# Kernel tuning notes

Measured on AMD Instinct MI355X. Metric: run time of the kernel, lower is better.

The kernel has to match this reference:

```python
import jax, jax.numpy as jnp
import numpy as np

_BN_EPS = 1e-5


def _conv2d(x, w, b, dilation):
    # x: (B,C,T,F), w: (O,I,k,k); 'same' padding per DilatedConv: (k-1)*d//2
    k = w.shape[-1]
    pad = (k - 1) * dilation // 2
    y = jax.lax.conv_general_dilated(
        x, w, window_strides=(1, 1),
        padding=[(pad, pad), (pad, pad)],
        rhs_dilation=(dilation, dilation),
        dimension_numbers=('NCHW', 'OIHW', 'NCHW'))
    return y + b[None, :, None, None]


def _gate(x, w, b, gamma, beta, mean, var, dilation):
    # conv -> BatchNorm2d (inference) -> chunk -> tanh * sigmoid
    y = _conv2d(x, w, b, dilation)
    scale = gamma * jax.lax.rsqrt(var + _BN_EPS)
    y = (y - mean[None, :, None, None]) * scale[None, :, None, None] + beta[None, :, None, None]
    a, g = jnp.split(y, 2, axis=1)
    return jnp.tanh(a) * jax.nn.sigmoid(g)


def _gru(x, wih, whh, bih, bhh):
    # forward-direction GRU (PyTorch gate order r,z,n). x: (T,N,I) -> (T,N,H)
    H = whh.shape[-1]
    gi = jnp.einsum('tni,hi->tnh', x, wih) + bih  # (T,N,3H), input projections

    def step(h, gi_t):
        gh = h @ whh.T + bhh
        r = jax.nn.sigmoid(gi_t[:, :H] + gh[:, :H])
        z = jax.nn.sigmoid(gi_t[:, H:2 * H] + gh[:, H:2 * H])
        n = jnp.tanh(gi_t[:, 2 * H:] + r * gh[:, 2 * H:])
        h_new = (1.0 - z) * n + z * h
        return h_new, h_new

    h0 = jnp.zeros((x.shape[1], H), x.dtype)
    _, ys = jax.lax.scan(step, h0, gi)
    return ys


def setup_inputs() -> dict:
    key = jax.random.key(0)
    ks = jax.random.split(key, 32)
    B, T, F, C, G = 8, 512, 256, 16, 8
    Cg = C // G  # 2
    d = {'x': jax.random.normal(ks[0], (B, 2, T, F), jnp.float32)}
    ki = 1
    for name, cin in zip(('g1', 'g2', 'g3', 'g4'), (2, C, C, C)):
        d[name + '_w'] = jax.random.normal(ks[ki], (2 * C, cin, 3, 3), jnp.float32) * (0.5 / np.sqrt(cin * 9.0)); ki += 1
        d[name + '_b'] = jax.random.normal(ks[ki], (2 * C,), jnp.float32) * 0.05; ki += 1
        d[name + '_gamma'] = 1.0 + 0.1 * jax.random.normal(ks[ki], (2 * C,), jnp.float32); ki += 1
        d[name + '_beta'] = 0.1 * jax.random.normal(ks[ki], (2 * C,), jnp.float32); ki += 1
        d[name + '_mean'] = jnp.zeros((2 * C,), jnp.float32)
        d[name + '_var'] = jnp.ones((2 * C,), jnp.float32)
    d['gru_wih'] = jax.random.normal(ks[ki], (G, 3 * Cg, Cg), jnp.float32) * 0.3; ki += 1
    d['gru_whh'] = jax.random.normal(ks[ki], (G, 3 * Cg, Cg), jnp.float32) * 0.3; ki += 1
    d['gru_bih'] = jax.random.normal(ks[ki], (G, 3 * Cg), jnp.float32) * 0.1; ki += 1
    d['gru_bhh'] = jax.random.normal(ks[ki], (G, 3 * Cg), jnp.float32) * 0.1; ki += 1
    d['out_w'] = jax.random.normal(ks[ki], (1, C), jnp.float32) * 0.3; ki += 1
    d['out_b'] = jax.random.normal(ks[ki], (1,), jnp.float32) * 0.05
    return d


def reference(x, g1_w, g1_b, g1_gamma, g1_beta, g1_mean, g1_var,
              g2_w, g2_b, g2_gamma, g2_beta, g2_mean, g2_var,
              g3_w, g3_b, g3_gamma, g3_beta, g3_mean, g3_var,
              g4_w, g4_b, g4_gamma, g4_beta, g4_mean, g4_var,
              gru_wih, gru_whh, gru_bih, gru_bhh, out_w, out_b):
    out = _gate(x, g1_w, g1_b, g1_gamma, g1_beta, g1_mean, g1_var, 1)
    out = _gate(out, g2_w, g2_b, g2_gamma, g2_beta, g2_mean, g2_var, 2)
    out = _gate(out, g3_w, g3_b, g3_gamma, g3_beta, g3_mean, g3_var, 4)
    out = _gate(out, g4_w, g4_b, g4_gamma, g4_beta, g4_mean, g4_var, 8)
    B, C, T, F = out.shape
    G = gru_wih.shape[0]
    Cg = C // G
    # split channels into G groups of Cg, run GRU over time, batched over (B*F)
    xg = out.reshape(B, G, Cg, T, F).transpose(1, 3, 0, 4, 2).reshape(G, T, B * F, Cg)
    ys = jax.vmap(_gru)(xg, gru_wih, gru_whh, gru_bih, gru_bhh)  # (G,T,B*F,Cg)
    merged = ys.reshape(G, T, B, F, Cg).transpose(2, 0, 4, 1, 3).reshape(B, C, T, F)
    # 1x1 out_conv -> 1 channel
    return jnp.einsum('bctf,oc->botf', merged, out_w) + out_b[None, :, None, None]
```

## Files before the change

kernel.cpp:

```cpp
#include <hip/hip_runtime.h>

#define Bb 8
#define Tt 512
#define Ff 256
#define Cc 16
#define TF (Tt*Ff)
#define TROW 528
#define FROW 272
#define CELL 32
#define WROWB (144*CELL)
#define BUFBYTES ((size_t)Bb*TROW*FROW*CELL)

typedef _Float16 half8 __attribute__((ext_vector_type(8)));
typedef __attribute__((ext_vector_type(4))) float f32x4;

typedef const __attribute__((address_space(1))) void* gas1_t;
typedef __attribute__((address_space(3))) void* las3_t;
#define GLOAD_LDS(g, l) __builtin_amdgcn_global_load_lds((gas1_t)(const void*)(g), (las3_t)(void*)(l), 16, 0, 0)

#define WAIT_VM8  0x0F78
#define WAIT_VM24 0x4F78
#define WAIT_VM40 0x8F78

__device__ __forceinline__ float fexp2(float x) { return __builtin_amdgcn_exp2f(x); }

__device__ __forceinline__ float fast_sigmoid(float x) {
    return __builtin_amdgcn_rcpf(1.0f + fexp2(-1.4426950408889634f * x));
}
__device__ __forceinline__ float fast_tanh(float x) {
    return 1.0f - 2.0f * __builtin_amdgcn_rcpf(fexp2(2.8853900817779268f * x) + 1.0f);
}

__device__ __forceinline__ unsigned short hbits(float x) {
    _Float16 h = (_Float16)x;
    return __builtin_bit_cast(unsigned short, h);
}
__device__ __forceinline__ float h2f(unsigned short u) {
    return (float)__builtin_bit_cast(_Float16, u);
}
__device__ __forceinline__ f32x4 mfma_f16(half8 a, half8 b, f32x4 c) {
    return __builtin_amdgcn_mfma_f32_16x16x32_f16(a, b, c, 0, 0, 0);
}
__device__ __forceinline__ float dpp_swap8(float x) {
    int xi = __builtin_bit_cast(int, x);
    int r = __builtin_amdgcn_mov_dpp(xi, 0x128, 0xf, 0xf, true);
    return __builtin_bit_cast(float, r);
}

__global__ __launch_bounds__(256)
void setup_all(const float* __restrict__ x1, const float* __restrict__ w1, const float* __restrict__ b1,
               const float* __restrict__ gm1, const float* __restrict__ bt1,
               const float* __restrict__ mn1, const float* __restrict__ vr1,
               const float* __restrict__ w2, const float* __restrict__ b2, const float* __restrict__ gm2,
               const float* __restrict__ bt2, const float* __restrict__ mn2, const float* __restrict__ vr2,
               const float* __restrict__ w3, const float* __restrict__ b3, const float* __restrict__ gm3,
               const float* __restrict__ bt3, const float* __restrict__ mn3, const float* __restrict__ vr3,
               const float* __restrict__ w4, const float* __restrict__ b4, const float* __restrict__ gm4,
               const float* __restrict__ bt4, const float* __restrict__ mn4, const float* __restrict__ vr4,
               char* __restrict__ bufA, char* __restrict__ bufB,
               char* __restrict__ wpreAll, float* __restrict__ bpreAll)
{
    const int blk = blockIdx.x;
    const int tid = threadIdx.x;
    if (blk < 3) {
        const float *w, *bias, *gamma, *beta, *mean, *var;
        if (blk == 0)      { w = w2; bias = b2; gamma = gm2; beta = bt2; mean = mn2; var = vr2; }
        else if (blk == 1) { w = w3; bias = b3; gamma = gm3; beta = bt3; mean = mn3; var = vr3; }
        else               { w = w4; bias = b4; gamma = gm4; beta = bt4; mean = mn4; var = vr4; }
        char* wpre = wpreAll + blk * 20480;
        float* bpre = bpreAll + blk * 32;
        if (tid < 32) {
            float s = gamma[tid] * rsqrtf(var[tid] + 1e-5f);
            bpre[tid] = (bias[tid] - mean[tid]) * s + beta[tid];
        }
        for (int i = tid; i < 4608; i += 256) {
            int co = i / 144, r = i - co * 144;
            int ci = r / 9, tap = r - ci * 9;
            float s = gamma[co] * rsqrtf(var[co] + 1e-5f);
            float wv = w[(co * 16 + ci) * 9 + tap] * s;
            unsigned short hi = hbits(wv);
            unsigned short lo = hbits((wv - h2f(hi)) * 2048.0f);
            int ks = tap >> 1, tp = tap & 1;
            int kl = tp * 16 + ci;
            int qq = kl >> 3, jj = kl & 7;
            int sub = qq ^ (co & 3);
            *(unsigned short*)(wpre + ((0 * 5 + ks) * 32 + co) * 64 + sub * 16 + jj * 2) = hi;
            *(unsigned short*)(wpre + ((1 * 5 + ks) * 32 + co) * 64 + sub * 16 + jj * 2) = lo;
        }
        for (int i = tid; i < 1024; i += 256) {
            int p = i >> 9, rem = i & 511;
            int co = rem >> 4, kl = 16 + (rem & 15);
            int qq = kl >> 3, jj = kl & 7;
            int sub = qq ^ (co & 3);
            *(unsigned short*)(wpre + ((p * 5 + 4) * 32 + co) * 64 + sub * 16 + jj * 2) = 0;
        }
    } else if (blk < 787) {
        int idx = (blk - 3) * 256 + tid;
        int which = idx >= 100352;
        int r0 = which ? idx - 100352 : idx;
        int b = r0 / 12544, c = r0 - b * 12544;
        int tp, fp;
        if (c < 4352) { int row = c / 272; fp = c - row * 272; tp = row < 8 ? row : 512 + row; }
        else { int c2 = c - 4352; tp = 8 + (c2 >> 4); int fi = c2 & 15; fp = fi < 8 ? fi : 256 + fi; }
        char* base = (which ? bufB : bufA) + ((size_t)(b * TROW + tp) * FROW + fp) * CELL;
        float4 z = make_float4(0.f, 0.f, 0.f, 0.f);
        float4* p = (float4*)base;
        p[0] = z; p[1] = z;
    } else {
        __shared__ float xs[2][6][66];
        __shared__ float wl[18 * 32];
        __shared__ float bnsL[32], bnoL[32];
        int bb = blk - 787;
        int fx = bb & 3;
        int ty = (bb >> 2) & 127;
        int b  = bb >> 9;
        const int f0 = fx * 64;
        const int t0 = ty * 4;
        const int fl = tid & 63;
        const int tr = (tid >> 6) & 1;
        const int h  = tid >> 7;

        if (tid < 32) {
            float s = gm1[tid] * rsqrtf(vr1[tid] + 1e-5f);
            bnsL[tid] = s;
            bnoL[tid] = (b1[tid] - mn1[tid]) * s + bt1[tid];
        }
        for (int i = tid; i < 576; i += 256) {
            int co = i & 31, rest = i >> 5;
            int ci = rest / 9, tap = rest - ci * 9;
            wl[rest * 32 + co] = w1[(co * 2 + ci) * 9 + tap];
        }
        for (int i = tid; i < 792; i += 256) {
            int ci = i / 396, r = i - ci * 396;
            int row = r / 66, col = r - row * 66;
            int t_in = t0 + row - 1, f_in = f0 + col - 1;
            float v = 0.f;
            if (t_in >= 0 && t_in < Tt && f_in >= 0 && f_in < Ff)
                v = x1[((size_t)(b * 2 + ci) * Tt + t_in) * Ff + f_in];
            xs[ci][row][col] = v;
        }
        __syncthreads();

        float acc[2][16];
        #pragma unroll
        for (int q = 0; q < 2; q++)
            #pragma unroll
            for (int j = 0; j < 16; j++) acc[q][j] = 0.f;

        #pragma unroll
        for (int ci = 0; ci < 2; ci++) {
            float win[4][3];
            #pragma unroll
            for (int r = 0; r < 4; r++)
                #pragma unroll
                for (int c = 0; c < 3; c++)
                    win[r][c] = xs[ci][2 * tr + r][fl + c];
            #pragma unroll
            for (int dt = 0; dt < 3; dt++)
                #pragma unroll
                for (int kf = 0; kf < 3; kf++) {
                    float xv0 = win[dt][kf];
                    float xv1 = win[dt + 1][kf];
                    const float* wrow = wl + (ci * 9 + dt * 3 + kf) * 32 + h * 8;
                    float wv[16];
                    *(float4*)(wv)      = *(const float4*)(wrow);
                    *(float4*)(wv + 4)  = *(const float4*)(wrow + 4);
                    *(float4*)(wv + 8)  = *(const float4*)(wrow + 16);
                    *(float4*)(wv + 12) = *(const float4*)(wrow + 20);
                    #pragma unroll
                    for (int j = 0; j < 16; j++) {
                        acc[0][j] = fmaf(xv0, wv[j], acc[0][j]);
                        acc[1][j] = fmaf(xv1, wv[j], acc[1][j]);
                    }
                }
        }

        #pragma unroll
        for (int q = 0; q < 2; q++) {
            int t = t0 + 2 * tr + q;
            int fp = f0 + fl + 8;
            int sw = fp & 1;
            char* cell = bufA + ((size_t)(b * TROW + t + 8) * FROW + fp) * CELL;
            unsigned short hv[8];
            #pragma unroll
            for (int j = 0; j < 8; j++) {
                int ca = h * 8 + j, cg = 16 + h * 8 + j;
                float av = acc[q][j]     * bnsL[ca] + bnoL[ca];
                float gv = acc[q][8 + j] * bnsL[cg] + bnoL[cg];
                hv[j] = hbits(fast_tanh(av) * fast_sigmoid(gv));
            }
            uint4 P;
            P.x = (unsigned)hv[0] | ((unsigned)hv[1] << 16);
            P.y = (unsigned)hv[2] | ((unsigned)hv[3] << 16);
            P.z = (unsigned)hv[4] | ((unsigned)hv[5] << 16);
            P.w = (unsigned)hv[6] | ((unsigned)hv[7] << 16);
            *(uint4*)(cell + ((h ^ sw) * 16)) = P;
        }
    }
}

template<int DIL, int WRITE_F32>
__global__ __launch_bounds__(256, 2)
void gate_mfma(const char* __restrict__ actIn, const char* __restrict__ wpre,
               const float* __restrict__ bpre, char* __restrict__ outBuf)
{
    __shared__ char actL[32768];
    const int tg = blockIdx.x, fh = blockIdx.y, b = blockIdx.z;
    const int tid = threadIdx.x;
    const int w = tid >> 6, lane = tid & 63;
    const int n = lane & 15, q = lane >> 4;
    const int tsel = w >> 1, fsel = w & 1;
    constexpr int GPC = 128 / DIL;
    const int rcl = tg / GPC, m = tg - rcl * GPC;
    const int t0 = rcl + 4 * m * DIL;
    const int f0 = fh * 128;

    half8 aH[5][2], aL[5][2];
    #pragma unroll
    for (int ks = 0; ks < 5; ks++)
        #pragma unroll
        for (int ct = 0; ct < 2; ct++) {
            int co = ct * 16 + n;
            int sub = q ^ (co & 3);
            aH[ks][ct] = *(const half8*)(wpre + (size_t)((0 * 5 + ks) * 32 + co) * 64 + sub * 16);
            aL[ks][ct] = *(const half8*)(wpre + (size_t)((5 + ks) * 32 + co) * 64 + sub * 16);
        }

    #pragma unroll
    for (int i = 0; i < 6; i++) {
        int tp = t0 + 8 + (i - 1) * DIL;
        const char* src = actIn + ((size_t)(b * TROW + tp) * FROW + f0) * CELL;
        char* dst = actL + i * WROWB;
        GLOAD_LDS(src + tid * 16, dst + tid * 16);
        if (tid < 64)
            GLOAD_LDS(src + (224 + tid) * 16, dst + (224 + tid) * 16);
    }
    __syncthreads();

    const int fbl = fsel * 64;
    f32x4 accH[2][4][2] = {}, accL[2][4][2] = {};

    #pragma unroll
    for (int ks = 0; ks < 5; ks++) {
        const int tapA = 2 * ks;
        const int tapB = (2 * ks + 1 > 8) ? 8 : 2 * ks + 1;
        const int rowA = tapA / 3, dfA = (tapA % 3 - 1) * DIL;
        const int rowB = tapB / 3, dfB = (tapB % 3 - 1) * DIL;
        int tapSel = q >> 1;
        int rowt = tapSel ? rowB : rowA;
        int df  = tapSel ? dfB : dfA;
        int cih = q & 1;
        #pragma unroll
        for (int tj = 0; tj < 2; tj++) {
            const int jj = 2 * tsel + tj;
            const char* rbase = actL + (jj + rowt) * WROWB;
            #pragma unroll
            for (int nt = 0; nt < 4; nt++) {
                int fp = 8 + fbl + nt * 16 + n + df;
                const char* cell = rbase + fp * CELL;
                half8 bF = *(const half8*)(cell + ((cih ^ (fp & 1)) * 16));
                #pragma unroll
                for (int ct = 0; ct < 2; ct++) {
                    accH[tj][nt][ct] = mfma_f16(aH[ks][ct], bF, accH[tj][nt][ct]);
                    accL[tj][nt][ct] = mfma_f16(aL[ks][ct], bF, accL[tj][nt][ct]);
                }
            }
        }
    }

    float4 bA = *(const float4*)(bpre + q * 4);
    float4 bG = *(const float4*)(bpre + 16 + q * 4);
    const float CL = 4.8828125e-4f;
    __syncthreads();

    if (WRITE_F32) {
        float* Ef = (float*)actL;
        #pragma unroll
        for (int tj = 0; tj < 2; tj++) {
            const int jj = 2 * tsel + tj;
            #pragma unroll
            for (int nt = 0; nt < 4; nt++) {
                float a0 = accH[tj][nt][0].x + CL * accL[tj][nt][0].x + bA.x;
                float a1 = accH[tj][nt][0].y + CL * accL[tj][nt][0].y + bA.y;
                float a2 = accH[tj][nt][0].z + CL * accL[tj][nt][0].z + bA.z;
                float a3 = accH[tj][nt][0].w + CL * accL[tj][nt][0].w + bA.w;
                float g0 = accH[tj][nt][1].x + CL * accL[tj][nt][1].x + bG.x;
                float g1 = accH[tj][nt][1].y + CL * accL[tj][nt][1].y + bG.y;
                float g2 = accH[tj][nt][1].z + CL * accL[tj][nt][1].z + bG.z;
                float g3 = accH[tj][nt][1].w + CL * accL[tj][nt][1].w + bG.w;
                float r[4];
                r[0] = fast_tanh(a0) * fast_sigmoid(g0);
                r[1] = fast_tanh(a1) * fast_sigmoid(g1);
                r[2] = fast_tanh(a2) * fast_sigmoid(g2);
                r[3] = fast_tanh(a3) * fast_sigmoid(g3);
                int fl = fbl + nt * 16 + n;
                #pragma unroll
                for (int j = 0; j < 4; j++)
                    Ef[(jj * 16 + q * 4 + j) * 128 + fl] = r[j];
            }
        }
        __syncthreads();
        float* gp = (float*)outBuf;
        #pragma unroll
        for (int k = 0; k < 8; k++) {
            int linear = k * 256 + tid;
            int jj2 = linear >> 9;
            int rem = linear & 511;
            int c = rem >> 5, fq = rem & 31;
            int tt = t0 + jj2 * DIL;
            *(float4*)(gp + (size_t)(b * 16 + c) * TF + tt * Ff + fh * 128 + fq * 4) =
                *(const float4*)(Ef + (jj2 * 16 + c) * 128 + fq * 4);
        }
    } else {
        char* Eo = actL;
        #pragma unroll
        for (int tj = 0; tj < 2; tj++) {
            const int jj = 2 * tsel + tj;
            #pragma unroll
            for (int nt = 0; nt < 4; nt++) {
                float a0 = accH[tj][nt][0].x + CL * accL[tj][nt][0].x + bA.x;
                float a1 = accH[tj][nt][0].y + CL * accL[tj][nt][0].y + bA.y;
                float a2 = accH[tj][nt][0].z + CL * accL[tj][nt][0].z + bA.z;
                float a3 = accH[tj][nt][0].w + CL * accL[tj][nt][0].w + bA.w;
                float g0 = accH[tj][nt][1].x + CL * accL[tj][nt][1].x + bG.x;
                float g1 = accH[tj][nt][1].y + CL * accL[tj][nt][1].y + bG.y;
                float g2 = accH[tj][nt][1].z + CL * accL[tj][nt][1].z + bG.z;
                float g3 = accH[tj][nt][1].w + CL * accL[tj][nt][1].w + bG.w;
                unsigned short hv[4];
                hv[0] = hbits(fast_tanh(a0) * fast_sigmoid(g0));
                hv[1] = hbits(fast_tanh(a1) * fast_sigmoid(g1));
                hv[2] = hbits(fast_tanh(a2) * fast_sigmoid(g2));
                hv[3] = hbits(fast_tanh(a3) * fast_sigmoid(g3));
                int fl = fbl + nt * 16 + n;
                int sw = (fh * 128 + fl + 8) & 1;
                uint2 pk;
                pk.x = (unsigned)hv[0] | ((unsigned)hv[1] << 16);
                pk.y = (unsigned)hv[2] | ((unsigned)hv[3] << 16);
                char* base = Eo + (jj * 128 + fl) * CELL;
                *(uint2*)(base + ((q >> 1) ^ sw) * 16 + (q & 1) * 8) = pk;
            }
        }
        __syncthreads();
        #pragma unroll
        for (int k = 0; k < 4; k++) {
            int linear = k * 256 + tid;
            int jj2 = linear >> 8;
            int idx = linear & 255;
            int tt = t0 + jj2 * DIL;
            char* dstRow = outBuf + ((size_t)(b * TROW + tt + 8) * FROW + fh * 128 + 8) * CELL;
            *(uint4*)(dstRow + idx * 16) = *(const uint4*)(Eo + jj2 * 4096 + idx * 16);
        }
    }
}

__global__ __launch_bounds__(128)
void gru_kernel(const float* __restrict__ xin, const float* __restrict__ wih,
                const float* __restrict__ whh, const float* __restrict__ bih,
                const float* __restrict__ bhh, const float* __restrict__ out_w,
                float* __restrict__ part)
{
    __shared__ float ldsF[2][3 * 2048];
    const int tid = threadIdx.x;
    const int wv = tid >> 6, lane = tid & 63;
    const int b = blockIdx.x >> 5;
    const int g = (blockIdx.x >> 2) & 7;
    const int fblk = (blockIdx.x & 3) * 2 + wv;
    const int f0 = fblk * 32;

    const int row = lane >> 4;
    const int u = (lane >> 3) & 1;
    const int fi = (lane & 7) | (row << 3);

    const float L2E = 1.4426950408889634f;
    float Wi0[3], Wi1[3], Whs[3], Who[3], Bi[3], Bh[3];
    #pragma unroll
    for (int p = 0; p < 3; p++) {
        int rw = p * 2 + u;
        Wi0[p] = wih[g * 12 + rw * 2 + 0] * L2E;
        Wi1[p] = wih[g * 12 + rw * 2 + 1] * L2E;
        Whs[p] = whh[g * 12 + rw * 2 + u] * L2E;
        Who[p] = whh[g * 12 + rw * 2 + (1 - u)] * L2E;
        Bi[p]  = bih[g * 6 + rw] * L2E;
        Bh[p]  = bhh[g * 6 + rw] * L2E;
    }
    const float ow = out_w[2 * g + u];

    const int s = lane & 7, cch = (lane >> 3) & 1, trr = lane >> 4;
    const float* gsrc = xin + ((size_t)(b * Cc + 2 * g + cch) * Tt + trr) * Ff + f0 + s * 4;
    float* ldsW = ldsF[wv];

    float* poW = part + ((((size_t)(b * 8 + g) * 8 + fblk) * 256) * 128) + u * 64 + fi * 2;

    #define STAGE(bsel, chunk)                                                 \
    {                                                                          \
        char* ldst = (char*)(ldsW + (bsel) * 2048) + lane * 16;                \
        const float* gs = gsrc + (size_t)(chunk) * 32 * Ff;                    \
        _Pragma("unroll")                                                      \
        for (int i = 0; i < 8; i++)                                            \
            GLOAD_LDS(gs + i * 4 * Ff, ldst + i * 1024);                       \
    }

    float h = 0.f;
    STAGE(0, 0); STAGE(1, 1);

    for (int k = 0; k < 16; k++) {
        __builtin_amdgcn_sched_barrier(0);
        if (k == 0)      __builtin_amdgcn_s_waitcnt(WAIT_VM8);
        else if (k == 1) __builtin_amdgcn_s_waitcnt(WAIT_VM24);
        else             __builtin_amdgcn_s_waitcnt(WAIT_VM40);
        __builtin_amdgcn_sched_barrier(0);
        int bc = k - (k / 3) * 3;
        const float* cbase = ldsW + bc * 2048;
        float2 outR[16];
        #pragma unroll
        for (int tt = 0; tt < 32; tt++) {
            const float* cell = cbase + (tt >> 2) * 256 + (tt & 3) * 64;
            float x0 = cell[fi];
            float x1 = cell[32 + fi];
            float ho = dpp_swap8(h);
            float gir = fmaf(Wi1[0], x1, fmaf(Wi0[0], x0, Bi[0]));
            float giz = fmaf(Wi1[1], x1, fmaf(Wi0[1], x0, Bi[1]));
            float gin = fmaf(Wi1[2], x1, fmaf(Wi0[2], x0, Bi[2]));
            float ghr = fmaf(Who[0], ho, fmaf(Whs[0], h, Bh[0]));
            float ghz = fmaf(Who[1], ho, fmaf(Whs[1], h, Bh[1]));
            float ghn = fmaf(Who[2], ho, fmaf(Whs[2], h, Bh[2]));
            float r = __builtin_amdgcn_rcpf(1.f + fexp2(-(gir + ghr)));
            float z = __builtin_amdgcn_rcpf(1.f + fexp2(-(giz + ghz)));
            float an = fmaf(r, ghn, gin);
            float nv = fmaf(-2.f, __builtin_amdgcn_rcpf(fexp2(an + an) + 1.f), 1.f);
            h = fmaf(z, h - nv, nv);
            float o = h * ow;
            if (tt & 1) outR[tt >> 1].y = o; else outR[tt >> 1].x = o;
        }
        int cs = k + 2; cs &= 15;
        int bs = k + 2; bs -= (bs / 3) * 3;
        STAGE(bs, cs);
        #pragma unroll
        for (int j = 0; j < 16; j++)
            *(float2*)(poW + (k * 16 + j) * 128) = outR[j];
    }
    #undef STAGE
}

__global__ __launch_bounds__(256)
void out_kernel(const float* __restrict__ part, const float* __restrict__ out_b,
                float* __restrict__ out)
{
    int idx = blockIdx.x * 256 + threadIdx.x;
    int f = idx & 255;
    int tp = (idx >> 8) & 255;
    int b = idx >> 16;
    int fsl = f >> 5, fi = f & 31;
    const float* base = part + (size_t)b * 2097152 + (size_t)fsl * 32768 + tp * 128 + fi * 2;
    float ob = out_b[0];
    float s0 = ob, s1 = ob;
    #pragma unroll
    for (int g = 0; g < 8; g++)
        #pragma unroll
        for (int u = 0; u < 2; u++) {
            float2 v = *(const float2*)(base + (size_t)g * 262144 + u * 64);
            s0 += v.x; s1 += v.y;
        }
    float* op = out + ((size_t)b * Tt + 2 * tp) * Ff + f;
    op[0] = s0;
    op[Ff] = s1;
}

extern "C" void kernel_launch(void* const* d_in, const int* in_sizes, int n_in,
                              void* d_out, int out_size, void* d_ws, size_t ws_size,
                              hipStream_t stream) {
    char* bufA = (char*)d_ws;
    char* bufB = bufA + BUFBYTES;
    float* gruF = (float*)(bufB + BUFBYTES);
    char* wpre = (char*)gruF + (size_t)Bb * Cc * TF * 4;
    float* bpre = (float*)(wpre + 3 * 20480);
    float* partF = (float*)bufA;

    setup_all<<<787 + 4096, 256, 0, stream>>>(
        (const float*)d_in[0],
        (const float*)d_in[1],  (const float*)d_in[2],  (const float*)d_in[3],
        (const float*)d_in[4],  (const float*)d_in[5],  (const float*)d_in[6],
        (const float*)d_in[7],  (const float*)d_in[8],  (const float*)d_in[9],
        (const float*)d_in[10], (const float*)d_in[11], (const float*)d_in[12],
        (const float*)d_in[13], (const float*)d_in[14], (const float*)d_in[15],
        (const float*)d_in[16], (const float*)d_in[17], (const float*)d_in[18],
        (const float*)d_in[19], (const float*)d_in[20], (const float*)d_in[21],
        (const float*)d_in[22], (const float*)d_in[23], (const float*)d_in[24],
        bufA, bufB, wpre, bpre);

    dim3 grid(128, 2, Bb), blk(256);
    gate_mfma<2, 0><<<grid, blk, 0, stream>>>(bufA, wpre,         bpre,      bufB);
    gate_mfma<4, 0><<<grid, blk, 0, stream>>>(bufB, wpre + 20480, bpre + 32, bufA);
    gate_mfma<8, 1><<<grid, blk, 0, stream>>>(bufA, wpre + 40960, bpre + 64, (char*)gruF);

    gru_kernel<<<256, 128, 0, stream>>>(
        gruF, (const float*)d_in[25], (const float*)d_in[26], (const float*)d_in[27],
        (const float*)d_in[28], (const float*)d_in[29], partF);

    out_kernel<<<2048, 256, 0, stream>>>(
        partF, (const float*)d_in[30], (float*)d_out);
}
```

Baseline: 273.6 us.

## Split gate MFMA into two accumulation passes and pre-reduce GRU outputs across lanes

The gate conv kernel now runs the low- and high-precision weight planes in two sequential passes over one accumulator set, scaling the accumulator between passes. This halves the accumulator registers and stops holding both weight sets live, so launch bounds can be raised to three blocks per CU. The GRU kernel sums the output projection across the paired lane with a DPP swap, so each lane writes half as many partials, and the final out_kernel reads half the data. Each lane also has fewer stores in flight, so the vmcnt wait threshold is lowered to match. The risks are a longer serial MFMA chain per pass, since the pass-1 scaling adds a dependency, and register spills under the tighter occupancy bound.

```diff
diff --git a/kernel.cpp b/kernel.cpp
--- a/kernel.cpp
+++ b/kernel.cpp
@@ -20,7 +20,7 @@
 
 #define WAIT_VM8  0x0F78
 #define WAIT_VM24 0x4F78
-#define WAIT_VM40 0x8F78
+#define WAIT_VM32 0x8F70
 
 __device__ __forceinline__ float fexp2(float x) { return __builtin_amdgcn_exp2f(x); }
 
@@ -200,7 +200,7 @@
 }
 
 template<int DIL, int WRITE_F32>
-__global__ __launch_bounds__(256, 2)
+__global__ __launch_bounds__(256, 3)
 void gate_mfma(const char* __restrict__ actIn, const char* __restrict__ wpre,
                const float* __restrict__ bpre, char* __restrict__ outBuf)
 {
@@ -215,17 +215,6 @@
     const int t0 = rcl + 4 * m * DIL;
     const int f0 = fh * 128;
 
-    half8 aH[5][2], aL[5][2];
-    #pragma unroll
-    for (int ks = 0; ks < 5; ks++)
-        #pragma unroll
-        for (int ct = 0; ct < 2; ct++) {
-            int co = ct * 16 + n;
-            int sub = q ^ (co & 3);
-            aH[ks][ct] = *(const half8*)(wpre + (size_t)((0 * 5 + ks) * 32 + co) * 64 + sub * 16);
-            aL[ks][ct] = *(const half8*)(wpre + (size_t)((5 + ks) * 32 + co) * 64 + sub * 16);
-        }
-
     #pragma unroll
     for (int i = 0; i < 6; i++) {
         int tp = t0 + 8 + (i - 1) * DIL;
@@ -238,61 +227,74 @@
     __syncthreads();
 
     const int fbl = fsel * 64;
-    f32x4 accH[2][4][2] = {}, accL[2][4][2] = {};
+    f32x4 acc[2][4][2] = {};
 
     #pragma unroll
-    for (int ks = 0; ks < 5; ks++) {
-        const int tapA = 2 * ks;
-        const int tapB = (2 * ks + 1 > 8) ? 8 : 2 * ks + 1;
-        const int rowA = tapA / 3, dfA = (tapA % 3 - 1) * DIL;
-        const int rowB = tapB / 3, dfB = (tapB % 3 - 1) * DIL;
-        int tapSel = q >> 1;
-        int rowt = tapSel ? rowB : rowA;
-        int df  = tapSel ? dfB : dfA;
-        int cih = q & 1;
+    for (int pass = 0; pass < 2; pass++) {
+        const int plane = 1 - pass;
+        half8 aw[5][2];
+        #pragma unroll
+        for (int ks = 0; ks < 5; ks++)
+            #pragma unroll
+            for (int ct = 0; ct < 2; ct++) {
+                int co = ct * 16 + n;
+                int sub = q ^ (co & 3);
+                aw[ks][ct] = *(const half8*)(wpre + (size_t)((plane * 5 + ks) * 32 + co) * 64 + sub * 16);
+            }
+        if (pass == 1) {
+            const float CLs = 4.8828125e-4f;
+            #pragma unroll
+            for (int tj = 0; tj < 2; tj++)
+                #pragma unroll
+                for (int nt = 0; nt < 4; nt++)
+                    #pragma unroll
+                    for (int ct = 0; ct < 2; ct++)
+                        acc[tj][nt][ct] *= CLs;
+        }
+        #pragma unroll
+        for (int ks = 0; ks < 5; ks++) {
+            const int tapA = 2 * ks;
+            const int tapB = (2 * ks + 1 > 8) ? 8 : 2 * ks + 1;
+            const int rowA = tapA / 3, dfA = (tapA % 3 - 1) * DIL;
+            const int rowB = tapB / 3, dfB = (tapB % 3 - 1) * DIL;
+            int tapSel = q >> 1;
+            int rowt = tapSel ? rowB : rowA;
+            int df  = tapSel ? dfB : dfA;
+            int cih = q & 1;
+            #pragma unroll
+            for (int tj = 0; tj < 2; tj++) {
+                const int jj = 2 * tsel + tj;
+                const char* rbase = actL + (jj + rowt) * WROWB;
+                #pragma unroll
+                for (int nt = 0; nt < 4; nt++) {
+                    int fp = 8 + fbl + nt * 16 + n + df;
+                    const char* cell = rbase + fp * CELL;
+                    half8 bF = *(const half8*)(cell + ((cih ^ (fp & 1)) * 16));
+                    #pragma unroll
+                    for (int ct = 0; ct < 2; ct++)
+                        acc[tj][nt][ct] = mfma_f16(aw[ks][ct], bF, acc[tj][nt][ct]);
+                }
+            }
+        }
+        __builtin_amdgcn_sched_barrier(0);
+    }
+
+    float4 bA = *(const float4*)(bpre + q * 4);
+    float4 bG = *(const float4*)(bpre + 16 + q * 4);
+    __syncthreads();
+
+    if (WRITE_F32) {
+        float* Ef = (float*)actL;
         #pragma unroll
         for (int tj = 0; tj < 2; tj++) {
             const int jj = 2 * tsel + tj;
-            const char* rbase = actL + (jj + rowt) * WROWB;
             #pragma unroll
             for (int nt = 0; nt < 4; nt++) {
-                int fp = 8 + fbl + nt * 16 + n + df;
-                const char* cell = rbase + fp * CELL;
-                half8 bF = *(const half8*)(cell + ((cih ^ (fp & 1)) * 16));
-                #pragma unroll
-                for (int ct = 0; ct < 2; ct++) {
-                    accH[tj][nt][ct] = mfma_f16(aH[ks][ct], bF, accH[tj][nt][ct]);
-                    accL[tj][nt][ct] = mfma_f16(aL[ks][ct], bF, accL[tj][nt][ct]);
-                }
-            }
-        }
-    }
-
-    float4 bA = *(const float4*)(bpre + q * 4);
-    float4 bG = *(const float4*)(bpre + 16 + q * 4);
-    const float CL = 4.8828125e-4f;
-    __syncthreads();
-
-    if (WRITE_F32) {
-        float* Ef = (float*)actL;
-        #pragma unroll
-        for (int tj = 0; tj < 2; tj++) {
-            const int jj = 2 * tsel + tj;
-            #pragma unroll
-            for (int nt = 0; nt < 4; nt++) {
-                float a0 = accH[tj][nt][0].x + CL * accL[tj][nt][0].x + bA.x;
-                float a1 = accH[tj][nt][0].y + CL * accL[tj][nt][0].y + bA.y;
-                float a2 = accH[tj][nt][0].z + CL * accL[tj][nt][0].z + bA.z;
-                float a3 = accH[tj][nt][0].w + CL * accL[tj][nt][0].w + bA.w;
-                float g0 = accH[tj][nt][1].x + CL * accL[tj][nt][1].x + bG.x;
-                float g1 = accH[tj][nt][1].y + CL * accL[tj][nt][1].y + bG.y;
-                float g2 = accH[tj][nt][1].z + CL * accL[tj][nt][1].z + bG.z;
-                float g3 = accH[tj][nt][1].w + CL * accL[tj][nt][1].w + bG.w;
                 float r[4];
-                r[0] = fast_tanh(a0) * fast_sigmoid(g0);
-                r[1] = fast_tanh(a1) * fast_sigmoid(g1);
-                r[2] = fast_tanh(a2) * fast_sigmoid(g2);
-                r[3] = fast_tanh(a3) * fast_sigmoid(g3);
+                r[0] = fast_tanh(acc[tj][nt][0].x + bA.x) * fast_sigmoid(acc[tj][nt][1].x + bG.x);
+                r[1] = fast_tanh(acc[tj][nt][0].y + bA.y) * fast_sigmoid(acc[tj][nt][1].y + bG.y);
+                r[2] = fast_tanh(acc[tj][nt][0].z + bA.z) * fast_sigmoid(acc[tj][nt][1].z + bG.z);
+                r[3] = fast_tanh(acc[tj][nt][0].w + bA.w) * fast_sigmoid(acc[tj][nt][1].w + bG.w);
                 int fl = fbl + nt * 16 + n;
                 #pragma unroll
                 for (int j = 0; j < 4; j++)
@@ -318,19 +320,11 @@
             const int jj = 2 * tsel + tj;
             #pragma unroll
             for (int nt = 0; nt < 4; nt++) {
-                float a0 = accH[tj][nt][0].x + CL * accL[tj][nt][0].x + bA.x;
-                float a1 = accH[tj][nt][0].y + CL * accL[tj][nt][0].y + bA.y;
-                float a2 = accH[tj][nt][0].z + CL * accL[tj][nt][0].z + bA.z;
-                float a3 = accH[tj][nt][0].w + CL * accL[tj][nt][0].w + bA.w;
-                float g0 = accH[tj][nt][1].x + CL * accL[tj][nt][1].x + bG.x;
-                float g1 = accH[tj][nt][1].y + CL * accL[tj][nt][1].y + bG.y;
-                float g2 = accH[tj][nt][1].z + CL * accL[tj][nt][1].z + bG.z;
-                float g3 = accH[tj][nt][1].w + CL * accL[tj][nt][1].w + bG.w;
                 unsigned short hv[4];
-                hv[0] = hbits(fast_tanh(a0) * fast_sigmoid(g0));
-                hv[1] = hbits(fast_tanh(a1) * fast_sigmoid(g1));
-                hv[2] = hbits(fast_tanh(a2) * fast_sigmoid(g2));
-                hv[3] = hbits(fast_tanh(a3) * fast_sigmoid(g3));
+                hv[0] = hbits(fast_tanh(acc[tj][nt][0].x + bA.x) * fast_sigmoid(acc[tj][nt][1].x + bG.x));
+                hv[1] = hbits(fast_tanh(acc[tj][nt][0].y + bA.y) * fast_sigmoid(acc[tj][nt][1].y + bG.y));
+                hv[2] = hbits(fast_tanh(acc[tj][nt][0].z + bA.z) * fast_sigmoid(acc[tj][nt][1].z + bG.z));
+                hv[3] = hbits(fast_tanh(acc[tj][nt][0].w + bA.w) * fast_sigmoid(acc[tj][nt][1].w + bG.w));
                 int fl = fbl + nt * 16 + n;
                 int sw = (fh * 128 + fl + 8) & 1;
                 uint2 pk;
@@ -389,7 +383,7 @@
     const float* gsrc = xin + ((size_t)(b * Cc + 2 * g + cch) * Tt + trr) * Ff + f0 + s * 4;
     float* ldsW = ldsF[wv];
 
-    float* poW = part + ((((size_t)(b * 8 + g) * 8 + fblk) * 256) * 128) + u * 64 + fi * 2;
+    float* poW = part + ((size_t)((b * 8 + g) * 8 + fblk)) * 16384 + fi * 2 + u * 512;
 
     #define STAGE(bsel, chunk)                                                 \
     {                                                                          \
@@ -407,7 +401,7 @@
         __builtin_amdgcn_sched_barrier(0);
         if (k == 0)      __builtin_amdgcn_s_waitcnt(WAIT_VM8);
         else if (k == 1) __builtin_amdgcn_s_waitcnt(WAIT_VM24);
-        else             __builtin_amdgcn_s_waitcnt(WAIT_VM40);
+        else             __builtin_amdgcn_s_waitcnt(WAIT_VM32);
         __builtin_amdgcn_sched_barrier(0);
         int bc = k - (k / 3) * 3;
         const float* cbase = ldsW + bc * 2048;
@@ -430,14 +424,17 @@
             float nv = fmaf(-2.f, __builtin_amdgcn_rcpf(fexp2(an + an) + 1.f), 1.f);
             h = fmaf(z, h - nv, nv);
             float o = h * ow;
-            if (tt & 1) outR[tt >> 1].y = o; else outR[tt >> 1].x = o;
+            float osum = o + dpp_swap8(o);
+            if (tt & 1) outR[tt >> 1].y = osum; else outR[tt >> 1].x = osum;
         }
         int cs = k + 2; cs &= 15;
         int bs = k + 2; bs -= (bs / 3) * 3;
         STAGE(bs, cs);
         #pragma unroll
-        for (int j = 0; j < 16; j++)
-            *(float2*)(poW + (k * 16 + j) * 128) = outR[j];
+        for (int j = 0; j < 8; j++) {
+            float2 val = u ? outR[j + 8] : outR[j];
+            *(float2*)(poW + (k * 16 + j) * 64) = val;
+        }
     }
     #undef STAGE
 }
@@ -450,17 +447,15 @@
     int f = idx & 255;
     int tp = (idx >> 8) & 255;
     int b = idx >> 16;
-    int fsl = f >> 5, fi = f & 31;
-    const float* base = part + (size_t)b * 2097152 + (size_t)fsl * 32768 + tp * 128 + fi * 2;
+    int fblk = f >> 5, fi = f & 31;
+    const float* base = part + (size_t)b * 1048576 + (size_t)fblk * 16384 + tp * 64 + fi * 2;
     float ob = out_b[0];
     float s0 = ob, s1 = ob;
     #pragma unroll
-    for (int g = 0; g < 8; g++)
-        #pragma unroll
-        for (int u = 0; u < 2; u++) {
-            float2 v = *(const float2*)(base + (size_t)g * 262144 + u * 64);
-            s0 += v.x; s1 += v.y;
-        }
+    for (int g = 0; g < 8; g++) {
+        float2 v = *(const float2*)(base + (size_t)g * 131072);
+        s0 += v.x; s1 += v.y;
+    }
     float* op = out + ((size_t)b * Tt + 2 * tp) * Ff + f;
     op[0] = s0;
     op[Ff] = s1;
```

Result: slower. 307.3 us (+12.3%).
